# Optimization experiments

Measured on AMD Instinct MI355X. Metric: run time of the kernel, lower is better.

## Reference

```python
import jax, jax.numpy as jnp
import numpy as np

NEG_SLOPE = 0.01  # torch nn.LeakyReLU default

B, N, IN_F, OUT_F, HEADS = 4, 2048, 512, 512, 8
D = OUT_F // HEADS  # 64


def setup_inputs() -> dict:
    key = jax.random.key(0)
    ks = jax.random.split(key, 4)
    X = jax.random.normal(ks[0], (B, N, IN_F), dtype=jnp.float32)
    W_v = jax.random.normal(ks[1], (IN_F, D), dtype=jnp.float32) * (IN_F ** -0.5)
    b_v = jnp.zeros((D,), dtype=jnp.float32)
    W_q = jax.random.normal(ks[2], (D, HEADS), dtype=jnp.float32) * (D ** -0.5)
    b_q = jnp.zeros((HEADS,), dtype=jnp.float32)
    W_k = jax.random.normal(ks[3], (D, HEADS), dtype=jnp.float32) * (D ** -0.5)
    b_k = jnp.zeros((HEADS,), dtype=jnp.float32)
    return {"X": X, "W_v": W_v, "b_v": b_v, "W_q": W_q, "b_q": b_q, "W_k": W_k, "b_k": b_k}


def reference(X, W_v, b_v, W_q, b_q, W_k, b_k):
    # V: (B, N, D)
    V = X @ W_v + b_v
    # per-node, per-head scalar scores: (B, N, H) -> (B, H, N)
    Q = jnp.swapaxes(V @ W_q + b_q, 1, 2)
    K = jnp.swapaxes(V @ W_k + b_k, 1, 2)
    # A[b,h,i,j] = leaky_relu(Q[b,h,j] + K[b,h,i])  (broadcast outer-sum)
    A = jax.nn.leaky_relu(Q[:, :, None, :] + K[:, :, :, None], negative_slope=NEG_SLOPE)
    A = jax.nn.softmax(A, axis=-1)  # dropout = identity in eval mode
    # H[b,i,h,f] = sum_j A[b,h,i,j] V[b,j,f]
    H = jnp.einsum('bhij,bjf->bihf', A, V)
    return H.reshape(H.shape[0], H.shape[1], -1)  # (B, N, H*D)
```

## Files before the change

kernel.cpp:

```cpp
#include <hip/hip_runtime.h>

#define BB   4
#define NN   2048
#define INF  512
#define HH   8
#define DD   64
#define BH   (BB*HH)
#define NCK  16
#define CKS  128
#define KSP  8


__global__ __launch_bounds__(128) void k_v(
    const float* __restrict__ X, const float* __restrict__ Wv,
    float* __restrict__ Vpart)
{
  __shared__ float Ws[64][68];
  const int t  = threadIdx.x;
  const int tc = t & 7;
  const int tr = t >> 3;
  const int rg = blockIdx.x >> 3;
  const int ks = blockIdx.x & 7;
  const int r0 = rg * 128;
  const int k0 = ks * 64;

  #pragma unroll
  for (int i = 0; i < 8; i++) {
    const int e4 = t + i * 128;
    const int k  = e4 >> 4;
    const int n4 = (e4 & 15) * 4;
    *(float4*)(&Ws[k][n4]) = *(const float4*)(Wv + (size_t)(k0 + k) * DD + n4);
  }
  __syncthreads();

  float acc[8][8] = {{0.f}};
  const float* xbase = X + (size_t)(r0 + tr * 8) * INF + k0;
  for (int kk = 0; kk < 64; kk += 4) {
    float4 xv[8];
    #pragma unroll
    for (int r = 0; r < 8; r++)
      xv[r] = *(const float4*)(xbase + (size_t)r * INF + kk);
    #pragma unroll
    for (int j = 0; j < 4; j++) {
      const float4 wa = *(const float4*)(&Ws[kk + j][tc * 8]);
      const float4 wb = *(const float4*)(&Ws[kk + j][tc * 8 + 4]);
      #pragma unroll
      for (int r = 0; r < 8; r++) {
        const float x = (j == 0) ? xv[r].x : (j == 1) ? xv[r].y : (j == 2) ? xv[r].z : xv[r].w;
        acc[r][0] += x * wa.x;  acc[r][1] += x * wa.y;
        acc[r][2] += x * wa.z;  acc[r][3] += x * wa.w;
        acc[r][4] += x * wb.x;  acc[r][5] += x * wb.y;
        acc[r][6] += x * wb.z;  acc[r][7] += x * wb.w;
      }
    }
  }
  float* vp = Vpart + ((size_t)ks * (BB*NN) + r0 + tr * 8) * DD + tc * 8;
  #pragma unroll
  for (int r = 0; r < 8; r++) {
    float4 oa, ob;
    oa.x = acc[r][0]; oa.y = acc[r][1]; oa.z = acc[r][2]; oa.w = acc[r][3];
    ob.x = acc[r][4]; ob.y = acc[r][5]; ob.z = acc[r][6]; ob.w = acc[r][7];
    *(float4*)(vp + (size_t)r * DD)     = oa;
    *(float4*)(vp + (size_t)r * DD + 4) = ob;
  }
}

__global__ __launch_bounds__(256) void k_vred(
    const float* __restrict__ Vpart, const float* __restrict__ bv,
    const float* __restrict__ Wq, const float* __restrict__ bq,
    const float* __restrict__ Wk, const float* __restrict__ bk,
    float* __restrict__ V, float* __restrict__ qsg, float* __restrict__ ksg)
{
  __shared__ float Vs[16][DD + 1];
  const int t  = threadIdx.x;
  const size_t e0 = ((size_t)blockIdx.x * 256 + t) * 4;
  const size_t STR = (size_t)BB * NN * DD;
  float4 a = *(const float4*)(Vpart + e0);
  #pragma unroll
  for (int p = 1; p < KSP; p++) {
    const float4 b = *(const float4*)(Vpart + (size_t)p * STR + e0);
    a.x += b.x;  a.y += b.y;  a.z += b.z;  a.w += b.w;
  }
  const float4 bb = *(const float4*)(bv + (e0 & 63));
  a.x += bb.x;  a.y += bb.y;  a.z += bb.z;  a.w += bb.w;
  *(float4*)(V + e0) = a;
  const int lrow = t >> 4;
  const int lcol = (t * 4) & 63;
  Vs[lrow][lcol]   = a.x;  Vs[lrow][lcol+1] = a.y;
  Vs[lrow][lcol+2] = a.z;  Vs[lrow][lcol+3] = a.w;
  __syncthreads();
  const int row = t >> 4;
  const int h   = t & 7;
  const bool isK = (t & 8) != 0;
  const float* W = isK ? Wk : Wq;
  float s = isK ? bk[h] : bq[h];
  #pragma unroll 8
  for (int dd = 0; dd < DD; dd++) s += Vs[row][dd] * W[dd*HH + h];
  const int grow = blockIdx.x * 16 + row;
  const int b = grow >> 11, n = grow & (NN - 1);
  (isK ? ksg : qsg)[(b*HH + h) * NN + n] = s;
}

__global__ __launch_bounds__(1024) void k_sort(
    float* __restrict__ q, unsigned short* __restrict__ idxg)
{
  __shared__ float key[NN];
  __shared__ int   idx[NN];
  const int t  = threadIdx.x;
  const int bh = blockIdx.x;
  key[t]        = q[bh*NN + t];        idx[t]        = t;
  key[t + 1024] = q[bh*NN + t + 1024]; idx[t + 1024] = t + 1024;
  __syncthreads();

#define CEX_STAGE(size, stride)                                         \
  {                                                                     \
    const int i = ((t & ~((stride) - 1)) << 1) | (t & ((stride) - 1));  \
    const int j = i + (stride);                                         \
    const bool up = ((i & (size)) == 0);                                \
    const float a = key[i], b = key[j];                                 \
    if (up ? (a > b) : (a < b)) {                                       \
      key[i] = b; key[j] = a;                                           \
      const int tmp = idx[i]; idx[i] = idx[j]; idx[j] = tmp;            \
    }                                                                   \
  }

  for (int size = 2; size <= 128; size <<= 1)
    for (int stride = size >> 1; stride > 0; stride >>= 1)
      CEX_STAGE(size, stride)
  __syncthreads();
  for (int size = 256; size <= 2048; size <<= 1) {
    for (int stride = size >> 1; stride >= 128; stride >>= 1) {
      CEX_STAGE(size, stride)
      __syncthreads();
    }
    for (int stride = 64; stride > 0; stride >>= 1)
      CEX_STAGE(size, stride)
    __syncthreads();
  }
#undef CEX_STAGE

  q[bh*NN + t]        = key[t];
  q[bh*NN + t + 1024] = key[t + 1024];
  idxg[bh*NN + t]        = (unsigned short)idx[t];
  idxg[bh*NN + t + 1024] = (unsigned short)idx[t + 1024];
}

__global__ __launch_bounds__(256) void k_scan(
    const float* __restrict__ sq, const unsigned short* __restrict__ idxg,
    const float* __restrict__ V,
    float* __restrict__ P1, float* __restrict__ P2,
    float* __restrict__ l1, float* __restrict__ l2,
    float* __restrict__ S1g, float* __restrict__ S2g,
    float* __restrict__ SL1, float* __restrict__ SL2)
{
  __shared__ float vstash[4][32][DD];
  __shared__ float ss1[4][64], ss2[4][64], sl1[4], sl2[4];
  const int t  = threadIdx.x;
  const int bh = blockIdx.x >> 4;
  const int ck = blockIdx.x & 15;
  const int d  = t & 63, g = t >> 6;
  const int r0 = ck*CKS + g*32;
  const float* Vb  = V + (size_t)(bh >> 3) * NN * DD;
  const float* sqb = sq + bh*NN;
  const unsigned short* ib = idxg + bh*NN;
  float a1 = 0.f, a2 = 0.f, s1 = 0.f, s2 = 0.f;
  #pragma unroll 8
  for (int rr = 0; rr < 32; rr++) {
    const int r = r0 + rr;
    const float qv = sqb[r];
    const float e1 = __expf(qv), e2 = __expf(0.01f*qv);
    const float v  = Vb[(size_t)ib[r]*DD + d];
    vstash[g][rr][d] = v;
    a1 += e1*v;  a2 += e2*v;  s1 += e1;  s2 += e2;
  }
  ss1[g][d] = a1;  ss2[g][d] = a2;
  if (d == 0) { sl1[g] = s1;  sl2[g] = s2; }
  __syncthreads();
  float o1 = 0.f, o2 = 0.f, lo1 = 0.f, lo2 = 0.f;
  for (int gg = 0; gg < g; gg++) { o1 += ss1[gg][d]; o2 += ss2[gg][d]; lo1 += sl1[gg]; lo2 += sl2[gg]; }
  if (g == 0) {
    S1g[(bh*NCK + ck)*64 + d] = ss1[0][d]+ss1[1][d]+ss1[2][d]+ss1[3][d];
    S2g[(bh*NCK + ck)*64 + d] = ss2[0][d]+ss2[1][d]+ss2[2][d]+ss2[3][d];
    if (d == 0) {
      SL1[bh*NCK + ck] = sl1[0]+sl1[1]+sl1[2]+sl1[3];
      SL2[bh*NCK + ck] = sl2[0]+sl2[1]+sl2[2]+sl2[3];
    }
  }
  a1 = o1; a2 = o2; s1 = lo1; s2 = lo2;
  float* P1b = P1 + (size_t)bh*NN*DD;
  float* P2b = P2 + (size_t)bh*NN*DD;
  #pragma unroll 8
  for (int rr = 0; rr < 32; rr++) {
    const int r = r0 + rr;
    const float qv = sqb[r];
    const float e1 = __expf(qv), e2 = __expf(0.01f*qv);
    const float v  = vstash[g][rr][d];
    P1b[(size_t)r*DD + d] = a1;
    P2b[(size_t)r*DD + d] = a2;
    if (d == 0) { l1[bh*NN + r] = s1;  l2[bh*NN + r] = s2; }
    a1 += e1*v;  a2 += e2*v;  s1 += e1;  s2 += e2;
  }
}

__global__ __launch_bounds__(256) void k_off(
    const float* __restrict__ S1g, const float* __restrict__ S2g,
    const float* __restrict__ SL1, const float* __restrict__ SL2,
    float* __restrict__ Off1, float* __restrict__ Off2,
    float* __restrict__ Loff1, float* __restrict__ Loff2)
{
  const int bh = blockIdx.x;
  const int t  = threadIdx.x;
  if (t < 128) {
    const int d = t & 63;
    const bool h2 = t >= 64;
    const float* S = h2 ? S2g : S1g;
    float* O = h2 ? Off2 : Off1;
    double a = 0.0;
    for (int ck = 0; ck < NCK; ck++) {
      O[((size_t)bh*(NCK+1) + ck)*64 + d] = (float)a;
      a += (double)S[((size_t)bh*NCK + ck)*64 + d];
    }
    O[((size_t)bh*(NCK+1) + NCK)*64 + d] = (float)a;
  } else if (t == 128 || t == 129) {
    const bool h2 = (t == 129);
    const float* S = h2 ? SL2 : SL1;
    float* O = h2 ? Loff2 : Loff1;
    double a = 0.0;
    for (int ck = 0; ck < NCK; ck++) { O[bh*(NCK+1) + ck] = (float)a; a += (double)S[bh*NCK + ck]; }
    O[bh*(NCK+1) + NCK] = (float)a;
  }
}

__global__ __launch_bounds__(256) void k_out(
    const float* __restrict__ sq, const float* __restrict__ ksg,
    const float* __restrict__ P1, const float* __restrict__ P2,
    const float* __restrict__ Off1, const float* __restrict__ Off2,
    const float* __restrict__ l1, const float* __restrict__ l2,
    const float* __restrict__ Loff1, const float* __restrict__ Loff2,
    float* __restrict__ out)
{
  const int t   = threadIdx.x;
  const int bh  = blockIdx.x >> 7;
  const int loc = blockIdx.x & 127;
  const int w   = t >> 6;
  const int d   = t & 63;
  const int i0  = loc*16 + w*4;
  const int b   = bh >> 3, h = bh & 7;
  const float* s = sq + bh*NN;
  const float probe = s[d*32 + 31];
  const float T1  = Off1[((size_t)bh*(NCK+1) + NCK)*64 + d];
  const float Lt1 = Loff1[bh*(NCK+1) + NCK];
  const size_t base = (size_t)bh * NN * DD;

  float kv[4], tt[4];
  int pos[4];
  #pragma unroll
  for (int u = 0; u < 4; u++) { kv[u] = ksg[bh*NN + i0 + u];  tt[u] = -kv[u]; }
  #pragma unroll
  for (int u = 0; u < 4; u++) {
    const unsigned long long m1 = __ballot(probe <= tt[u]);
    const int c1 = __popcll(m1);
    if (c1 == 64) pos[u] = NN;
    else {
      const unsigned long long m2 = __ballot(s[c1*32 + (d & 31)] <= tt[u]);
      pos[u] = c1*32 + (__popcll(m2) >> 1);
    }
  }
  #pragma unroll
  for (int u = 0; u < 4; u++) {
    const float ek  = __expf(kv[u]);
    const float ek2 = __expf(0.01f * kv[u]);
    float p1v, p2v, q1v, q2v;
    if (pos[u] < NN) {
      const int ch = pos[u] >> 7;
      p1v = P1[base + (size_t)pos[u]*DD + d] + Off1[((size_t)bh*(NCK+1) + ch)*64 + d];
      p2v = P2[base + (size_t)pos[u]*DD + d] + Off2[((size_t)bh*(NCK+1) + ch)*64 + d];
      q1v = l1[bh*NN + pos[u]] + Loff1[bh*(NCK+1) + ch];
      q2v = l2[bh*NN + pos[u]] + Loff2[bh*(NCK+1) + ch];
    } else {
      p1v = T1;   p2v = Off2[((size_t)bh*(NCK+1) + NCK)*64 + d];
      q1v = Lt1;  q2v = Loff2[bh*(NCK+1) + NCK];
    }
    const float num = ek * (T1 - p1v)  + ek2 * p2v;
    const float den = ek * (Lt1 - q1v) + ek2 * q2v;
    out[((size_t)(b*NN + i0 + u)) * (HH*DD) + h*DD + d] = num / den;
  }
}

extern "C" void kernel_launch(void* const* d_in, const int* in_sizes, int n_in,
                              void* d_out, int out_size, void* d_ws, size_t ws_size,
                              hipStream_t stream)
{
  (void)in_sizes; (void)n_in; (void)out_size; (void)ws_size;
  const float* X  = (const float*)d_in[0];
  const float* Wv = (const float*)d_in[1];
  const float* bv = (const float*)d_in[2];
  const float* Wq = (const float*)d_in[3];
  const float* bq = (const float*)d_in[4];
  const float* Wk = (const float*)d_in[5];
  const float* bk = (const float*)d_in[6];
  float* out = (float*)d_out;

  float* w = (float*)d_ws;
  float* V     = w;  w += (size_t)BB*NN*DD;
  float* qsg   = w;  w += BH*NN;
  float* ksg   = w;  w += BH*NN;
  float* l1    = w;  w += BH*NN;
  float* l2    = w;  w += BH*NN;
  unsigned short* idxg = (unsigned short*)w;  w += BH*NN/2;
  float* Off1  = w;  w += BH*(NCK+1)*DD;
  float* Off2  = w;  w += BH*(NCK+1)*DD;
  float* Loff1 = w;  w += BH*(NCK+1);
  float* Loff2 = w;  w += BH*(NCK+1);
  float* P1    = w;  w += (size_t)BH*NN*DD;
  float* P2    = w;  w += (size_t)BH*NN*DD;

  float* Vpart = P1;

  float* S1g = out;
  float* S2g = S1g + BH*NCK*DD;
  float* SL1 = S2g + BH*NCK*DD;
  float* SL2 = SL1 + BH*NCK;

  k_v    <<<512, 128, 0, stream>>>(X, Wv, Vpart);
  k_vred <<<512, 256, 0, stream>>>(Vpart, bv, Wq, bq, Wk, bk, V, qsg, ksg);
  k_sort <<<BH, 1024, 0, stream>>>(qsg, idxg);
  k_scan <<<BH*NCK, 256, 0, stream>>>(qsg, idxg, V, P1, P2, l1, l2, S1g, S2g, SL1, SL2);
  k_off  <<<BH, 256, 0, stream>>>(S1g, S2g, SL1, SL2, Off1, Off2, Loff1, Loff2);
  k_out  <<<BH*128, 256, 0, stream>>>(qsg, ksg, P1, P2, Off1, Off2, l1, l2, Loff1, Loff2, out);
}
```

Measured before the change: 145.8 us.

## Fuse chunk-offset prefix into output kernel and reduce split-K in V projection

Removes the separate k_off launch by having each k_out block compute the per-chunk prefix offsets for its (b,h) into shared memory, replacing the global Off arrays. The partial-sum buffers move from the output buffer into the workspace. The V projection kernel is retiled from 8 K-splits of 128-row tiles to 2 K-splits of 32-row tiles with 256 threads, which cuts the partial-sum traffic reduced by k_vred. Trade-offs: the prefix is recomputed redundantly in every k_out block and now accumulates in float instead of double, and k_v loses per-thread register reuse.

```diff
diff --git a/kernel.cpp b/kernel.cpp
--- a/kernel.cpp
+++ b/kernel.cpp
@@ -8,60 +8,56 @@
 #define BH   (BB*HH)
 #define NCK  16
 #define CKS  128
-#define KSP  8
-
-
-__global__ __launch_bounds__(128) void k_v(
+#define KSP  2
+
+
+__global__ __launch_bounds__(256) void k_v(
     const float* __restrict__ X, const float* __restrict__ Wv,
     float* __restrict__ Vpart)
 {
   __shared__ float Ws[64][68];
   const int t  = threadIdx.x;
-  const int tc = t & 7;
-  const int tr = t >> 3;
-  const int rg = blockIdx.x >> 3;
-  const int ks = blockIdx.x & 7;
-  const int r0 = rg * 128;
-  const int k0 = ks * 64;
-
-  #pragma unroll
-  for (int i = 0; i < 8; i++) {
-    const int e4 = t + i * 128;
-    const int k  = e4 >> 4;
-    const int n4 = (e4 & 15) * 4;
-    *(float4*)(&Ws[k][n4]) = *(const float4*)(Wv + (size_t)(k0 + k) * DD + n4);
-  }
-  __syncthreads();
-
-  float acc[8][8] = {{0.f}};
-  const float* xbase = X + (size_t)(r0 + tr * 8) * INF + k0;
-  for (int kk = 0; kk < 64; kk += 4) {
-    float4 xv[8];
+  const int tc = t & 15;
+  const int tr = t >> 4;
+  const int rg = blockIdx.x >> 1;
+  const int kh = blockIdx.x & 1;
+  const int r0 = rg * 32;
+  const int k0 = kh * 256;
+  float acc[2][4] = {{0.f}};
+
+  for (int kc = 0; kc < 256; kc += 64) {
+    __syncthreads();
     #pragma unroll
-    for (int r = 0; r < 8; r++)
-      xv[r] = *(const float4*)(xbase + (size_t)r * INF + kk);
-    #pragma unroll
-    for (int j = 0; j < 4; j++) {
-      const float4 wa = *(const float4*)(&Ws[kk + j][tc * 8]);
-      const float4 wb = *(const float4*)(&Ws[kk + j][tc * 8 + 4]);
+    for (int i = 0; i < 4; i++) {
+      const int e4 = t + i * 256;
+      const int k  = e4 >> 4;
+      const int n4 = (e4 & 15) * 4;
+      *(float4*)(&Ws[k][n4]) = *(const float4*)(Wv + (size_t)(k0 + kc + k) * DD + n4);
+    }
+    __syncthreads();
+    const float* xp0 = X + (size_t)(r0 + tr * 2) * INF + k0 + kc;
+    const float* xp1 = xp0 + INF;
+    #pragma unroll 8
+    for (int kk = 0; kk < 64; kk += 4) {
+      const float4 xa = *(const float4*)(xp0 + kk);
+      const float4 xb = *(const float4*)(xp1 + kk);
       #pragma unroll
-      for (int r = 0; r < 8; r++) {
-        const float x = (j == 0) ? xv[r].x : (j == 1) ? xv[r].y : (j == 2) ? xv[r].z : xv[r].w;
-        acc[r][0] += x * wa.x;  acc[r][1] += x * wa.y;
-        acc[r][2] += x * wa.z;  acc[r][3] += x * wa.w;
-        acc[r][4] += x * wb.x;  acc[r][5] += x * wb.y;
-        acc[r][6] += x * wb.z;  acc[r][7] += x * wb.w;
+      for (int j = 0; j < 4; j++) {
+        const float4 w4 = *(const float4*)(&Ws[kk + j][tc * 4]);
+        const float xaj = (j == 0) ? xa.x : (j == 1) ? xa.y : (j == 2) ? xa.z : xa.w;
+        const float xbj = (j == 0) ? xb.x : (j == 1) ? xb.y : (j == 2) ? xb.z : xb.w;
+        acc[0][0] += xaj * w4.x;  acc[0][1] += xaj * w4.y;
+        acc[0][2] += xaj * w4.z;  acc[0][3] += xaj * w4.w;
+        acc[1][0] += xbj * w4.x;  acc[1][1] += xbj * w4.y;
+        acc[1][2] += xbj * w4.z;  acc[1][3] += xbj * w4.w;
       }
     }
   }
-  float* vp = Vpart + ((size_t)ks * (BB*NN) + r0 + tr * 8) * DD + tc * 8;
-  #pragma unroll
-  for (int r = 0; r < 8; r++) {
-    float4 oa, ob;
-    oa.x = acc[r][0]; oa.y = acc[r][1]; oa.z = acc[r][2]; oa.w = acc[r][3];
-    ob.x = acc[r][4]; ob.y = acc[r][5]; ob.z = acc[r][6]; ob.w = acc[r][7];
-    *(float4*)(vp + (size_t)r * DD)     = oa;
-    *(float4*)(vp + (size_t)r * DD + 4) = ob;
+  float* vp = Vpart + ((size_t)kh * (BB*NN) + r0 + tr * 2) * DD + tc * 4;
+  #pragma unroll
+  for (int r = 0; r < 2; r++) {
+    float4 o;  o.x = acc[r][0];  o.y = acc[r][1];  o.z = acc[r][2];  o.w = acc[r][3];
+    *(float4*)(vp + (size_t)r * DD) = o;
   }
 }
 
@@ -202,43 +198,16 @@
   }
 }
 
-__global__ __launch_bounds__(256) void k_off(
-    const float* __restrict__ S1g, const float* __restrict__ S2g,
-    const float* __restrict__ SL1, const float* __restrict__ SL2,
-    float* __restrict__ Off1, float* __restrict__ Off2,
-    float* __restrict__ Loff1, float* __restrict__ Loff2)
-{
-  const int bh = blockIdx.x;
-  const int t  = threadIdx.x;
-  if (t < 128) {
-    const int d = t & 63;
-    const bool h2 = t >= 64;
-    const float* S = h2 ? S2g : S1g;
-    float* O = h2 ? Off2 : Off1;
-    double a = 0.0;
-    for (int ck = 0; ck < NCK; ck++) {
-      O[((size_t)bh*(NCK+1) + ck)*64 + d] = (float)a;
-      a += (double)S[((size_t)bh*NCK + ck)*64 + d];
-    }
-    O[((size_t)bh*(NCK+1) + NCK)*64 + d] = (float)a;
-  } else if (t == 128 || t == 129) {
-    const bool h2 = (t == 129);
-    const float* S = h2 ? SL2 : SL1;
-    float* O = h2 ? Loff2 : Loff1;
-    double a = 0.0;
-    for (int ck = 0; ck < NCK; ck++) { O[bh*(NCK+1) + ck] = (float)a; a += (double)S[bh*NCK + ck]; }
-    O[bh*(NCK+1) + NCK] = (float)a;
-  }
-}
-
 __global__ __launch_bounds__(256) void k_out(
     const float* __restrict__ sq, const float* __restrict__ ksg,
     const float* __restrict__ P1, const float* __restrict__ P2,
-    const float* __restrict__ Off1, const float* __restrict__ Off2,
+    const float* __restrict__ S1g, const float* __restrict__ S2g,
+    const float* __restrict__ SL1, const float* __restrict__ SL2,
     const float* __restrict__ l1, const float* __restrict__ l2,
-    const float* __restrict__ Loff1, const float* __restrict__ Loff2,
     float* __restrict__ out)
 {
+  __shared__ float Of1[NCK + 1][64], Of2[NCK + 1][64];
+  __shared__ float Lo1[NCK + 1], Lo2[NCK + 1];
   const int t   = threadIdx.x;
   const int bh  = blockIdx.x >> 7;
   const int loc = blockIdx.x & 127;
@@ -246,10 +215,35 @@
   const int d   = t & 63;
   const int i0  = loc*16 + w*4;
   const int b   = bh >> 3, h = bh & 7;
+
+  if (t < 64) {
+    float a = 0.f;
+    for (int ck = 0; ck < NCK; ck++) {
+      Of1[ck][t] = a;  a += S1g[(bh*NCK + ck)*64 + t];
+    }
+    Of1[NCK][t] = a;
+  } else if (t < 128) {
+    const int dd = t - 64;
+    float a = 0.f;
+    for (int ck = 0; ck < NCK; ck++) {
+      Of2[ck][dd] = a;  a += S2g[(bh*NCK + ck)*64 + dd];
+    }
+    Of2[NCK][dd] = a;
+  } else if (t == 128) {
+    float a = 0.f;
+    for (int ck = 0; ck < NCK; ck++) { Lo1[ck] = a;  a += SL1[bh*NCK + ck]; }
+    Lo1[NCK] = a;
+  } else if (t == 129) {
+    float a = 0.f;
+    for (int ck = 0; ck < NCK; ck++) { Lo2[ck] = a;  a += SL2[bh*NCK + ck]; }
+    Lo2[NCK] = a;
+  }
+  __syncthreads();
+
   const float* s = sq + bh*NN;
   const float probe = s[d*32 + 31];
-  const float T1  = Off1[((size_t)bh*(NCK+1) + NCK)*64 + d];
-  const float Lt1 = Loff1[bh*(NCK+1) + NCK];
+  const float T1  = Of1[NCK][d];
+  const float Lt1 = Lo1[NCK];
   const size_t base = (size_t)bh * NN * DD;
 
   float kv[4], tt[4];
@@ -273,13 +267,13 @@
     float p1v, p2v, q1v, q2v;
     if (pos[u] < NN) {
       const int ch = pos[u] >> 7;
-      p1v = P1[base + (size_t)pos[u]*DD + d] + Off1[((size_t)bh*(NCK+1) + ch)*64 + d];
-      p2v = P2[base + (size_t)pos[u]*DD + d] + Off2[((size_t)bh*(NCK+1) + ch)*64 + d];
-      q1v = l1[bh*NN + pos[u]] + Loff1[bh*(NCK+1) + ch];
-      q2v = l2[bh*NN + pos[u]] + Loff2[bh*(NCK+1) + ch];
+      p1v = P1[base + (size_t)pos[u]*DD + d] + Of1[ch][d];
+      p2v = P2[base + (size_t)pos[u]*DD + d] + Of2[ch][d];
+      q1v = l1[bh*NN + pos[u]] + Lo1[ch];
+      q2v = l2[bh*NN + pos[u]] + Lo2[ch];
     } else {
-      p1v = T1;   p2v = Off2[((size_t)bh*(NCK+1) + NCK)*64 + d];
-      q1v = Lt1;  q2v = Loff2[bh*(NCK+1) + NCK];
+      p1v = T1;   p2v = Of2[NCK][d];
+      q1v = Lt1;  q2v = Lo2[NCK];
     }
     const float num = ek * (T1 - p1v)  + ek2 * p2v;
     const float den = ek * (Lt1 - q1v) + ek2 * q2v;
@@ -308,24 +302,18 @@
   float* l1    = w;  w += BH*NN;
   float* l2    = w;  w += BH*NN;
   unsigned short* idxg = (unsigned short*)w;  w += BH*NN/2;
-  float* Off1  = w;  w += BH*(NCK+1)*DD;
-  float* Off2  = w;  w += BH*(NCK+1)*DD;
-  float* Loff1 = w;  w += BH*(NCK+1);
-  float* Loff2 = w;  w += BH*(NCK+1);
+  float* S1g   = w;  w += (size_t)BH*NCK*DD;
+  float* S2g   = w;  w += (size_t)BH*NCK*DD;
+  float* SL1   = w;  w += BH*NCK;
+  float* SL2   = w;  w += BH*NCK;
   float* P1    = w;  w += (size_t)BH*NN*DD;
   float* P2    = w;  w += (size_t)BH*NN*DD;
 
   float* Vpart = P1;
 
-  float* S1g = out;
-  float* S2g = S1g + BH*NCK*DD;
-  float* SL1 = S2g + BH*NCK*DD;
-  float* SL2 = SL1 + BH*NCK;
-
-  k_v    <<<512, 128, 0, stream>>>(X, Wv, Vpart);
+  k_v    <<<512, 256, 0, stream>>>(X, Wv, Vpart);
   k_vred <<<512, 256, 0, stream>>>(Vpart, bv, Wq, bq, Wk, bk, V, qsg, ksg);
   k_sort <<<BH, 1024, 0, stream>>>(qsg, idxg);
   k_scan <<<BH*NCK, 256, 0, stream>>>(qsg, idxg, V, P1, P2, l1, l2, S1g, S2g, SL1, SL2);
-  k_off  <<<BH, 256, 0, stream>>>(S1g, S2g, SL1, SL2, Off1, Off2, Loff1, Loff2);
-  k_out  <<<BH*128, 256, 0, stream>>>(qsg, ksg, P1, P2, Off1, Off2, l1, l2, Loff1, Loff2, out);
-}
+  k_out  <<<BH*128, 256, 0, stream>>>(qsg, ksg, P1, P2, S1g, S2g, SL1, SL2, l1, l2, out);
+}
```

Result: faster. 138.3 us (-5.2%).
